# Kernel optimization log

Hardware: AMD Instinct MI355X
Metric: run time of the kernel (lower is better)

Reference implementation:

```python
import jax, jax.numpy as jnp
import numpy as np

SIGMA = 5.67e-8  # Stefan-Boltzmann constant
NX = 13
N = NX * NX  # 169 nodes
B = 131072


def _build_matrices(L=0.1, thickness=0.001, board_k=15.0, emis=0.8):
    dx = L / (NX - 1)
    dy = L / (NX - 1)
    GLx = thickness * board_k * dy / dx
    GLy = thickness * board_k * dx / dy
    GR = 2.0 * dx * dy * emis
    iface = {0, NX - 1, NX * NX - 1, NX * NX - NX}
    K = np.zeros((N, N), dtype=np.float32)
    for j in range(NX):
        for i in range(NX):
            idn = i + NX * j
            if idn in iface:
                K[idn, idn] = 1.0
            else:
                gii = 0.0
                if i + 1 < NX:
                    K[idn, idn + 1] = -GLx  # east
                    gii += GLx
                if i - 1 >= 0:
                    K[idn, idn - 1] = -GLx  # west
                    gii += GLx
                if j + 1 < NX:
                    K[idn, idn + NX] = -GLx  # north (original code uses -GLx here too)
                    gii += GLy
                if j - 1 >= 0:
                    K[idn, idn - NX] = -GLx  # south (original code uses -GLx here too)
                    gii += GLy
                K[idn, idn] = gii
    e = np.full(N, GR, dtype=np.float32)
    for t in iface:
        e[t] = 0.0
    return jnp.asarray(K), jnp.asarray(e)


def setup_inputs() -> dict:
    key = jax.random.key(0)
    k1, k2, k3, k4 = jax.random.split(key, 4)
    # realistic temperatures (K) and heat loads (W)
    outputs = 270.0 + 60.0 * jax.random.uniform(k1, (B, NX, NX), dtype=jnp.float32)
    heaters = 0.5 * jax.random.uniform(k2, (B, NX, NX), dtype=jnp.float32)
    interfaces = 0.5 * jax.random.uniform(k3, (B, NX, NX), dtype=jnp.float32)
    Tenv = 270.0 + 30.0 * jax.random.uniform(k4, (B, 1), dtype=jnp.float32)
    K, e_diag = _build_matrices()
    return {"outputs": outputs, "heaters": heaters, "interfaces": interfaces,
            "Tenv": Tenv, "K": K, "e_diag": e_diag}


def reference(outputs, heaters, interfaces, Tenv, K, e_diag):
    b = outputs.shape[0]
    T = outputs.reshape(b, -1)                    # [B, 169]
    Q = heaters.reshape(b, -1) + interfaces.reshape(b, -1)  # [B, 169]
    # original computes K @ T_nodes_x_batch; batch-major equivalent is T @ K^T
    conduction = jnp.einsum('bn,mn->bm', T, K)    # [B, 169]
    radiation = SIGMA * e_diag[None, :] * (T ** 4 - Tenv ** 4)  # Tenv [B,1] broadcasts
    excess = conduction + radiation - Q
    return jnp.mean(jnp.abs(excess))
```

## Files before the change

kernel.cpp:

```cpp
#include <hip/hip_runtime.h>
#include <math.h>


#define SIGMA_F 5.67e-8f

constexpr int BLOCK = 256;

typedef float f4a __attribute__((ext_vector_type(4), aligned(4)));
typedef float f4b __attribute__((ext_vector_type(4), aligned(16)));

__global__ __launch_bounds__(256) void fused_residual_v8(
    const float* __restrict__ T,
    const float* __restrict__ H,
    const float* __restrict__ F,
    const float* __restrict__ Tenv,
    const float* __restrict__ K,
    const float* __restrict__ Ediag,
    float* __restrict__ partials,
    int total)
{
    __shared__ unsigned sTab[184];
    __shared__ float sred[BLOCK / 64];

    const float GLx = -K[1 * 169 + 2];
    const float GRs = SIGMA_F * Ediag[1];

    const int tid  = (int)threadIdx.x;
    const int lane = tid & 63;

    if (tid < 184) {
        int m = (tid < 169) ? tid : tid - 169;
        int ii = m % 13;
        unsigned cW = (ii > 0)  ? 1u : 0u;
        unsigned cE = (ii < 12) ? 1u : 0u;
        unsigned cN = (m < 156) ? 1u : 0u;
        unsigned cS = (m >= 13) ? 1u : 0u;
        sTab[tid] = cW | (cE << 8) | (cN << 16) | (cS << 24);
    }
    __syncthreads();

    float acc = 0.0f;

    const int gstride = gridDim.x * BLOCK;
    for (int g = blockIdx.x * BLOCK + tid; g * 16 < total; g += gstride) {
        const int e0 = g * 16;
        const int waveBase = e0 - lane * 16;
        const bool fast = (waveBase >= 16) && (waveBase + 64 * 16 + 32 <= total);

        if (fast) {
            f4b t0 = *(const f4b*)(T + e0);
            f4b t1 = *(const f4b*)(T + e0 + 4);
            f4b t2 = *(const f4b*)(T + e0 + 8);
            f4b t3 = *(const f4b*)(T + e0 + 12);
            f4b h0 = __builtin_nontemporal_load((const f4b*)(H + e0));
            f4b h1 = __builtin_nontemporal_load((const f4b*)(H + e0 + 4));
            f4b h2 = __builtin_nontemporal_load((const f4b*)(H + e0 + 8));
            f4b h3 = __builtin_nontemporal_load((const f4b*)(H + e0 + 12));
            f4b f0 = __builtin_nontemporal_load((const f4b*)(F + e0));
            f4b f1 = __builtin_nontemporal_load((const f4b*)(F + e0 + 4));
            f4b f2 = __builtin_nontemporal_load((const f4b*)(F + e0 + 8));
            f4b f3 = __builtin_nontemporal_load((const f4b*)(F + e0 + 12));

            f4a pa, pb, pc; float pd = 0.0f;
            if (lane == 0) {
                pa = *(const f4a*)(T + e0 - 13);
                pb = *(const f4a*)(T + e0 - 9);
                pc = *(const f4a*)(T + e0 - 5);
                pd = T[e0 - 1];
            }
            f4a na, nb, nc; float nd = 0.0f;
            if (lane == 63) {
                na = *(const f4a*)(T + e0 + 16);
                nb = *(const f4a*)(T + e0 + 20);
                nc = *(const f4a*)(T + e0 + 24);
                nd = T[e0 + 28];
            }

            const float tR[16] = {t0.x, t0.y, t0.z, t0.w, t1.x, t1.y, t1.z, t1.w,
                                  t2.x, t2.y, t2.z, t2.w, t3.x, t3.y, t3.z, t3.w};

            float sv[16];
            sv[13] = tR[0]; sv[14] = tR[1]; sv[15] = tR[2];
            #pragma unroll
            for (int j = 0; j < 13; ++j) sv[j] = __shfl_up(tR[j + 3], 1);
            float nv[16];
            nv[0] = tR[13]; nv[1] = tR[14]; nv[2] = tR[15];
            #pragma unroll
            for (int j = 3; j < 16; ++j) nv[j] = __shfl_down(tR[j - 3], 1);

            float left  = __shfl_up(tR[15], 1);
            float right = __shfl_down(tR[0], 1);

            if (lane == 0) {
                sv[0] = pa.x; sv[1] = pa.y; sv[2]  = pa.z; sv[3]  = pa.w;
                sv[4] = pb.x; sv[5] = pb.y; sv[6]  = pb.z; sv[7]  = pb.w;
                sv[8] = pc.x; sv[9] = pc.y; sv[10] = pc.z; sv[11] = pc.w;
                sv[12] = pd;  left = pd;
            }
            if (lane == 63) {
                nv[3]  = na.x; nv[4]  = na.y; nv[5]  = na.z; nv[6]  = na.w;
                nv[7]  = nb.x; nv[8]  = nb.y; nv[9]  = nb.z; nv[10] = nb.w;
                nv[11] = nc.x; nv[12] = nc.y; nv[13] = nc.z; nv[14] = nc.w;
                nv[15] = nd;   right = na.x;
            }

            const unsigned ue = (unsigned)e0;
            const unsigned b0 = ue / 169u;
            const int m0 = (int)(ue - b0 * 169u);

            float tvA = Tenv[b0];
            float tvB = tvA;
            if (m0 >= 154) tvB = Tenv[b0 + 1];
            const float tv4A = (tvA * tvA) * (tvA * tvA);
            const float tv4B = (tvB * tvB) * (tvB * tvB);

            const float qv[16] = {h0.x + f0.x, h0.y + f0.y, h0.z + f0.z, h0.w + f0.w,
                                  h1.x + f1.x, h1.y + f1.y, h1.z + f1.z, h1.w + f1.w,
                                  h2.x + f2.x, h2.y + f2.y, h2.z + f2.z, h2.w + f2.w,
                                  h3.x + f3.x, h3.y + f3.y, h3.z + f3.z, h3.w + f3.w};

            #pragma unroll
            for (int j = 0; j < 16; ++j) {
                const unsigned w = sTab[m0 + j];
                const float mW = (float)(w & 0xffu);
                const float mE = (float)((w >> 8) & 0xffu);
                const float mN = (float)((w >> 16) & 0xffu);
                const float mS = (float)(w >> 24);

                const float t  = tR[j];
                const float tw = (j == 0)  ? left  : tR[j - 1];
                const float te = (j == 15) ? right : tR[j + 1];
                float s = mW * tw;
                s = fmaf(mE, te, s);
                s = fmaf(mN, nv[j], s);
                s = fmaf(mS, sv[j], s);
                const float nn = (mW + mE) + (mN + mS);
                const float q  = qv[j];
                const float tv4 = (m0 + j >= 169) ? tv4B : tv4A;
                const float t2 = t * t;
                const float d  = fmaf(t2, t2, -tv4);
                const float core = fmaf(GLx, fmaf(nn, t, -s), fmaf(GRs, d, -q));
                const float ex = (nn == 2.0f) ? (t - q) : core;
                acc += fabsf(ex);
            }
        } else {
            #pragma unroll
            for (int j = 0; j < 16; ++j) {
                int e = e0 + j;
                if (e >= total) break;
                unsigned b = (unsigned)e / 169u;
                int m = e - (int)b * 169;
                unsigned q13 = (unsigned)m / 13u;
                int ii = m - (int)q13 * 13;
                bool cE = (ii < 12), cW = (ii > 0), cN = (m < 156), cS = (m >= 13);
                bool ifc = (m == 0) | (m == 12) | (m == 156) | (m == 168);
                float t  = T[e];
                float tEv = cE ? T[e + 1]  : 0.0f;
                float tWv = cW ? T[e - 1]  : 0.0f;
                float tNv = cN ? T[e + 13] : 0.0f;
                float tSv = cS ? T[e - 13] : 0.0f;
                float s  = tEv + tWv + tNv + tSv;
                float nn = (float)((int)cE + (int)cW + (int)cN + (int)cS);
                float tv = Tenv[b];
                float tv4 = (tv * tv) * (tv * tv);
                float t2 = t * t, t4 = t2 * t2;
                float qq = H[e] + F[e];
                float ex = ifc ? (t - qq)
                               : (GLx * (nn * t - s) + GRs * (t4 - tv4) - qq);
                acc += fabsf(ex);
            }
        }
    }

    #pragma unroll
    for (int off = 32; off > 0; off >>= 1)
        acc += __shfl_down(acc, off, 64);
    const int wid = tid >> 6;
    if (lane == 0) sred[wid] = acc;
    __syncthreads();
    if (tid == 0) {
        float s = 0.0f;
        #pragma unroll
        for (int w = 0; w < BLOCK / 64; ++w) s += sred[w];
        partials[blockIdx.x] = s;
    }
}

__global__ __launch_bounds__(256) void finalize_kernel(
    const float* __restrict__ partials, int n,
    float* __restrict__ out, float inv_total)
{
    __shared__ float sred[BLOCK / 64];
    float acc = 0.0f;
    for (int i = (int)threadIdx.x; i < n; i += BLOCK) acc += partials[i];
    #pragma unroll
    for (int off = 32; off > 0; off >>= 1)
        acc += __shfl_down(acc, off, 64);
    int lane = threadIdx.x & 63;
    int wid  = threadIdx.x >> 6;
    if (lane == 0) sred[wid] = acc;
    __syncthreads();
    if (threadIdx.x == 0) {
        float s = 0.0f;
        #pragma unroll
        for (int w = 0; w < BLOCK / 64; ++w) s += sred[w];
        out[0] = s * inv_total;
    }
}

extern "C" void kernel_launch(void* const* d_in, const int* in_sizes, int n_in,
                              void* d_out, int out_size, void* d_ws, size_t ws_size,
                              hipStream_t stream) {
    const float* T    = (const float*)d_in[0];
    const float* H    = (const float*)d_in[1];
    const float* F    = (const float*)d_in[2];
    const float* Tenv = (const float*)d_in[3];
    const float* K    = (const float*)d_in[4];
    const float* E    = (const float*)d_in[5];
    float* out      = (float*)d_out;
    float* partials = (float*)d_ws;

    const int total = in_sizes[0];

    int grid = (total / 16 + BLOCK - 1) / BLOCK;
    if ((size_t)grid * sizeof(float) > ws_size) grid = (int)(ws_size / sizeof(float));
    if (grid < 1) grid = 1;

    fused_residual_v8<<<grid, BLOCK, 0, stream>>>(T, H, F, Tenv, K, E, partials, total);

    const float inv_total = 1.0f / (float)total;
    finalize_kernel<<<1, BLOCK, 0, stream>>>(partials, grid, out, inv_total);
}
```

Before: 254.2 us.

## Stage tiles into LDS with double-buffered async global_load_lds in persistent blocks

```diff
diff --git a/kernel.cpp b/kernel.cpp
--- a/kernel.cpp
+++ b/kernel.cpp
@@ -1,15 +1,24 @@
 #include <hip/hip_runtime.h>
 #include <math.h>
+#include <stdint.h>
 
 
 #define SIGMA_F 5.67e-8f
 
 constexpr int BLOCK = 256;
-
-typedef float f4a __attribute__((ext_vector_type(4), aligned(4)));
+constexpr int TILE  = 2048;
+constexpr int THALO = 16;
+constexpr int TWIN  = TILE + 2 * THALO;
+
 typedef float f4b __attribute__((ext_vector_type(4), aligned(16)));
 
-__global__ __launch_bounds__(256) void fused_residual_v8(
+static __device__ __forceinline__ void gl_lds16(const float* g, float* l) {
+    __builtin_amdgcn_global_load_lds(
+        (const __attribute__((address_space(1))) void*)g,
+        (__attribute__((address_space(3))) void*)l, 16, 0, 0);
+}
+
+__global__ __launch_bounds__(256) void fused_residual_v9(
     const float* __restrict__ T,
     const float* __restrict__ H,
     const float* __restrict__ F,
@@ -17,16 +26,18 @@
     const float* __restrict__ K,
     const float* __restrict__ Ediag,
     float* __restrict__ partials,
-    int total)
+    int total,
+    int ntiles)
 {
+    __shared__ float sT[2][TWIN];
+    __shared__ float sH[2][TILE];
+    __shared__ float sF[2][TILE];
     __shared__ unsigned sTab[184];
     __shared__ float sred[BLOCK / 64];
 
     const float GLx = -K[1 * 169 + 2];
     const float GRs = SIGMA_F * Ediag[1];
-
-    const int tid  = (int)threadIdx.x;
-    const int lane = tid & 63;
+    const int tid = (int)threadIdx.x;
 
     if (tid < 184) {
         int m = (tid < 169) ? tid : tid - 169;
@@ -37,72 +48,68 @@
         unsigned cS = (m >= 13) ? 1u : 0u;
         sTab[tid] = cW | (cE << 8) | (cN << 16) | (cS << 24);
     }
-    __syncthreads();
+
+    const int nb  = (int)gridDim.x;
+    const int bid = (int)blockIdx.x;
+    const int qd  = ntiles / nb, rem = ntiles % nb;
+    const int t0  = bid * qd + (bid < rem ? bid : rem);
+    const int nt  = qd + (bid < rem ? 1 : 0);
 
     float acc = 0.0f;
 
-    const int gstride = gridDim.x * BLOCK;
-    for (int g = blockIdx.x * BLOCK + tid; g * 16 < total; g += gstride) {
-        const int e0 = g * 16;
-        const int waveBase = e0 - lane * 16;
-        const bool fast = (waveBase >= 16) && (waveBase + 64 * 16 + 32 <= total);
-
-        if (fast) {
-            f4b t0 = *(const f4b*)(T + e0);
-            f4b t1 = *(const f4b*)(T + e0 + 4);
-            f4b t2 = *(const f4b*)(T + e0 + 8);
-            f4b t3 = *(const f4b*)(T + e0 + 12);
-            f4b h0 = __builtin_nontemporal_load((const f4b*)(H + e0));
-            f4b h1 = __builtin_nontemporal_load((const f4b*)(H + e0 + 4));
-            f4b h2 = __builtin_nontemporal_load((const f4b*)(H + e0 + 8));
-            f4b h3 = __builtin_nontemporal_load((const f4b*)(H + e0 + 12));
-            f4b f0 = __builtin_nontemporal_load((const f4b*)(F + e0));
-            f4b f1 = __builtin_nontemporal_load((const f4b*)(F + e0 + 4));
-            f4b f2 = __builtin_nontemporal_load((const f4b*)(F + e0 + 8));
-            f4b f3 = __builtin_nontemporal_load((const f4b*)(F + e0 + 12));
-
-            f4a pa, pb, pc; float pd = 0.0f;
-            if (lane == 0) {
-                pa = *(const f4a*)(T + e0 - 13);
-                pb = *(const f4a*)(T + e0 - 9);
-                pc = *(const f4a*)(T + e0 - 5);
-                pd = T[e0 - 1];
+    auto STAGE = [&](int buf, int tile) {
+        const int gb = tile * TILE;
+        #pragma unroll
+        for (int k = 0; k < 3; ++k) {
+            const int c = tid + k * BLOCK;
+            if (c < TWIN / 4) {
+                int src = gb - THALO + c * 4;
+                src = src < 0 ? 0 : src;
+                src = src > total - 4 ? total - 4 : src;
+                gl_lds16(T + src, &sT[buf][c * 4]);
             }
-            f4a na, nb, nc; float nd = 0.0f;
-            if (lane == 63) {
-                na = *(const f4a*)(T + e0 + 16);
-                nb = *(const f4a*)(T + e0 + 20);
-                nc = *(const f4a*)(T + e0 + 24);
-                nd = T[e0 + 28];
-            }
-
-            const float tR[16] = {t0.x, t0.y, t0.z, t0.w, t1.x, t1.y, t1.z, t1.w,
-                                  t2.x, t2.y, t2.z, t2.w, t3.x, t3.y, t3.z, t3.w};
-
-            float sv[16];
-            sv[13] = tR[0]; sv[14] = tR[1]; sv[15] = tR[2];
-            #pragma unroll
-            for (int j = 0; j < 13; ++j) sv[j] = __shfl_up(tR[j + 3], 1);
-            float nv[16];
-            nv[0] = tR[13]; nv[1] = tR[14]; nv[2] = tR[15];
-            #pragma unroll
-            for (int j = 3; j < 16; ++j) nv[j] = __shfl_down(tR[j - 3], 1);
-
-            float left  = __shfl_up(tR[15], 1);
-            float right = __shfl_down(tR[0], 1);
-
-            if (lane == 0) {
-                sv[0] = pa.x; sv[1] = pa.y; sv[2]  = pa.z; sv[3]  = pa.w;
-                sv[4] = pb.x; sv[5] = pb.y; sv[6]  = pb.z; sv[7]  = pb.w;
-                sv[8] = pc.x; sv[9] = pc.y; sv[10] = pc.z; sv[11] = pc.w;
-                sv[12] = pd;  left = pd;
-            }
-            if (lane == 63) {
-                nv[3]  = na.x; nv[4]  = na.y; nv[5]  = na.z; nv[6]  = na.w;
-                nv[7]  = nb.x; nv[8]  = nb.y; nv[9]  = nb.z; nv[10] = nb.w;
-                nv[11] = nc.x; nv[12] = nc.y; nv[13] = nc.z; nv[14] = nc.w;
-                nv[15] = nd;   right = na.x;
-            }
+        }
+        #pragma unroll
+        for (int k = 0; k < 2; ++k) {
+            const int c = tid + k * BLOCK;
+            gl_lds16(H + gb + c * 4, &sH[buf][c * 4]);
+            gl_lds16(F + gb + c * 4, &sF[buf][c * 4]);
+        }
+    };
+
+    if (nt > 0) {
+        STAGE(0, t0);
+        __syncthreads();
+        int cur = 0;
+        for (int k = 0; k < nt; ++k) {
+            if (k + 1 < nt) STAGE(cur ^ 1, t0 + k + 1);
+
+            const int tb = (t0 + k) * TILE;
+            const int e0 = tb + tid * 8;
+            const int lb = THALO + tid * 8;
+            const float* __restrict__ Tb = &sT[cur][0];
+
+            f4b a0 = *(const f4b*)&Tb[lb];
+            f4b a1 = *(const f4b*)&Tb[lb + 4];
+            float s0 = Tb[lb - 13];
+            f4b sA = *(const f4b*)&Tb[lb - 12];
+            f4b sB = *(const f4b*)&Tb[lb - 8];
+            float n0 = Tb[lb + 13], n1 = Tb[lb + 14], n2 = Tb[lb + 15];
+            f4b nA = *(const f4b*)&Tb[lb + 16];
+            float n7 = Tb[lb + 20];
+            float tw = Tb[lb - 1], te = Tb[lb + 8];
+            f4b h0v = *(const f4b*)&sH[cur][tid * 8];
+            f4b h1v = *(const f4b*)&sH[cur][tid * 8 + 4];
+            f4b f0v = *(const f4b*)&sF[cur][tid * 8];
+            f4b f1v = *(const f4b*)&sF[cur][tid * 8 + 4];
+
+            const float tC[8] = {a0.x, a0.y, a0.z, a0.w, a1.x, a1.y, a1.z, a1.w};
+            const float sv[8] = {s0, sA.x, sA.y, sA.z, sA.w, sB.x, sB.y, sB.z};
+            const float nv[8] = {n0, n1, n2, nA.x, nA.y, nA.z, nA.w, n7};
+            const float qv[8] = {h0v.x + f0v.x, h0v.y + f0v.y,
+                                 h0v.z + f0v.z, h0v.w + f0v.w,
+                                 h1v.x + f1v.x, h1v.y + f1v.y,
+                                 h1v.z + f1v.z, h1v.w + f1v.w};
 
             const unsigned ue = (unsigned)e0;
             const unsigned b0 = ue / 169u;
@@ -110,28 +117,23 @@
 
             float tvA = Tenv[b0];
             float tvB = tvA;
-            if (m0 >= 154) tvB = Tenv[b0 + 1];
+            if (m0 >= 162) tvB = Tenv[b0 + 1];
             const float tv4A = (tvA * tvA) * (tvA * tvA);
             const float tv4B = (tvB * tvB) * (tvB * tvB);
 
-            const float qv[16] = {h0.x + f0.x, h0.y + f0.y, h0.z + f0.z, h0.w + f0.w,
-                                  h1.x + f1.x, h1.y + f1.y, h1.z + f1.z, h1.w + f1.w,
-                                  h2.x + f2.x, h2.y + f2.y, h2.z + f2.z, h2.w + f2.w,
-                                  h3.x + f3.x, h3.y + f3.y, h3.z + f3.z, h3.w + f3.w};
-
             #pragma unroll
-            for (int j = 0; j < 16; ++j) {
+            for (int j = 0; j < 8; ++j) {
                 const unsigned w = sTab[m0 + j];
                 const float mW = (float)(w & 0xffu);
                 const float mE = (float)((w >> 8) & 0xffu);
                 const float mN = (float)((w >> 16) & 0xffu);
                 const float mS = (float)(w >> 24);
 
-                const float t  = tR[j];
-                const float tw = (j == 0)  ? left  : tR[j - 1];
-                const float te = (j == 15) ? right : tR[j + 1];
-                float s = mW * tw;
-                s = fmaf(mE, te, s);
+                const float t  = tC[j];
+                const float twv = (j == 0) ? tw : tC[j - 1];
+                const float tev = (j == 7) ? te : tC[j + 1];
+                float s = mW * twv;
+                s = fmaf(mE, tev, s);
                 s = fmaf(mN, nv[j], s);
                 s = fmaf(mS, sv[j], s);
                 const float nn = (mW + mE) + (mN + mS);
@@ -143,46 +145,43 @@
                 const float ex = (nn == 2.0f) ? (t - q) : core;
                 acc += fabsf(ex);
             }
-        } else {
-            #pragma unroll
-            for (int j = 0; j < 16; ++j) {
-                int e = e0 + j;
-                if (e >= total) break;
-                unsigned b = (unsigned)e / 169u;
-                int m = e - (int)b * 169;
-                unsigned q13 = (unsigned)m / 13u;
-                int ii = m - (int)q13 * 13;
-                bool cE = (ii < 12), cW = (ii > 0), cN = (m < 156), cS = (m >= 13);
-                bool ifc = (m == 0) | (m == 12) | (m == 156) | (m == 168);
-                float t  = T[e];
-                float tEv = cE ? T[e + 1]  : 0.0f;
-                float tWv = cW ? T[e - 1]  : 0.0f;
-                float tNv = cN ? T[e + 13] : 0.0f;
-                float tSv = cS ? T[e - 13] : 0.0f;
-                float s  = tEv + tWv + tNv + tSv;
-                float nn = (float)((int)cE + (int)cW + (int)cN + (int)cS);
-                float tv = Tenv[b];
-                float tv4 = (tv * tv) * (tv * tv);
-                float t2 = t * t, t4 = t2 * t2;
-                float qq = H[e] + F[e];
-                float ex = ifc ? (t - qq)
-                               : (GLx * (nn * t - s) + GRs * (t4 - tv4) - qq);
-                acc += fabsf(ex);
-            }
+
+            __syncthreads();
+            cur ^= 1;
         }
+    }
+
+    for (int e = ntiles * TILE + bid * BLOCK + tid; e < total;
+         e += nb * BLOCK) {
+        unsigned b = (unsigned)e / 169u;
+        int m = e - (int)b * 169;
+        int ii = m % 13;
+        bool cE = (ii < 12), cW = (ii > 0), cN = (m < 156), cS = (m >= 13);
+        bool ifc = (m == 0) | (m == 12) | (m == 156) | (m == 168);
+        float t  = T[e];
+        float s  = (cE ? T[e + 1] : 0.0f) + (cW ? T[e - 1] : 0.0f)
+                 + (cN ? T[e + 13] : 0.0f) + (cS ? T[e - 13] : 0.0f);
+        float nn = (float)((int)cE + (int)cW + (int)cN + (int)cS);
+        float tv = Tenv[b];
+        float tv4 = (tv * tv) * (tv * tv);
+        float t2 = t * t, t4 = t2 * t2;
+        float qq = H[e] + F[e];
+        float ex = ifc ? (t - qq) : (GLx * (nn * t - s) + GRs * (t4 - tv4) - qq);
+        acc += fabsf(ex);
     }
 
     #pragma unroll
     for (int off = 32; off > 0; off >>= 1)
         acc += __shfl_down(acc, off, 64);
-    const int wid = tid >> 6;
+    const int lane = tid & 63;
+    const int wid  = tid >> 6;
     if (lane == 0) sred[wid] = acc;
     __syncthreads();
     if (tid == 0) {
         float s = 0.0f;
         #pragma unroll
         for (int w = 0; w < BLOCK / 64; ++w) s += sred[w];
-        partials[blockIdx.x] = s;
+        partials[bid] = s;
     }
 }
 
@@ -220,13 +219,16 @@
     float* out      = (float*)d_out;
     float* partials = (float*)d_ws;
 
-    const int total = in_sizes[0];
-
-    int grid = (total / 16 + BLOCK - 1) / BLOCK;
+    const int total  = in_sizes[0];
+    const int ntiles = total / TILE;
+
+    int grid = 768;
+    if (grid > ntiles) grid = ntiles > 0 ? ntiles : 1;
     if ((size_t)grid * sizeof(float) > ws_size) grid = (int)(ws_size / sizeof(float));
     if (grid < 1) grid = 1;
 
-    fused_residual_v8<<<grid, BLOCK, 0, stream>>>(T, H, F, Tenv, K, E, partials, total);
+    fused_residual_v9<<<grid, BLOCK, 0, stream>>>(T, H, F, Tenv, K, E, partials,
+                                                  total, ntiles);
 
     const float inv_total = 1.0f / (float)total;
     finalize_kernel<<<1, BLOCK, 0, stream>>>(partials, grid, out, inv_total);
```

New measurement: 268.3 us. 1.06x slower.
